# Kernel optimization log

Hardware: AMD Instinct MI355X
Metric: run time of the kernel (lower is better)

The kernel has to match this reference:

```python
import math
import jax, jax.numpy as jnp
import numpy as np

N, T, C = 4, 2048, 1024
H, HS = 16, 64  # n_head, head_size; attention_dim = H*HS = 1024
LAYER_ID, N_LAYERS = 1, 12
_EPS = math.exp(-LAYER_ID / N_LAYERS)
EPS_R = _EPS / 2.0
EPS_K = _EPS + 0.3 * LAYER_ID / (N_LAYERS - 1)
EPS_V = _EPS


def setup_inputs() -> dict:
    key = jax.random.key(0)
    ks = jax.random.split(key, 9)
    s = 1.0 / math.sqrt(C)
    return {
        "x":  jax.random.normal(ks[0], (N, T, C), dtype=jnp.float32),
        "Wr": jax.random.normal(ks[1], (H * HS, C), dtype=jnp.float32) * s,
        "br": jax.random.normal(ks[2], (H * HS,), dtype=jnp.float32) * 0.01,
        "Wk": jax.random.normal(ks[3], (H * HS, C), dtype=jnp.float32) * s,
        "bk": jax.random.normal(ks[4], (H * HS,), dtype=jnp.float32) * 0.01,
        "Wv": jax.random.normal(ks[5], (H * HS, C), dtype=jnp.float32) * s,
        "bv": jax.random.normal(ks[6], (H * HS,), dtype=jnp.float32) * 0.01,
        "Wo": jax.random.normal(ks[7], (C, H * HS), dtype=jnp.float32) * s,
        "bo": jax.random.normal(ks[8], (C,), dtype=jnp.float32) * 0.01,
        "time_decay": jnp.full((H * HS,), 0.1, dtype=jnp.float32),
        "U":          jnp.full((H * HS,), 0.1, dtype=jnp.float32),
    }


def _time_interp(x, eps):
    # eps * x[t-1] + (1-eps) * x[t+1], zero-padded at the ends (ZeroPad2d semantics)
    Tn = x.shape[1]
    curr = jnp.pad(x, ((0, 0), (1, 0), (0, 0)))[:, :Tn]   # shift right: row t <- x[t-1]
    prev = jnp.pad(x, ((0, 0), (0, 1), (0, 0)))[:, 1:]    # shift left:  row t <- x[t+1]
    return eps * curr + (1.0 - eps) * prev


def reference(x, Wr, br, Wk, bk, Wv, bv, Wo, bo, time_decay, U):
    n, t, c = x.shape
    R = (_time_interp(x, EPS_R) @ Wr.T + br).reshape(n, t, H, HS)
    K = (_time_interp(x, EPS_K) @ Wk.T + bk).reshape(n, t, H, HS)
    V = (_time_interp(x, EPS_V) @ Wv.T + bv).reshape(n, t, H, HS)

    w = jax.nn.relu(time_decay).reshape(1, 1, H, HS)
    t_rem = (t - jnp.arange(1, t + 1, dtype=x.dtype)).reshape(1, t, 1, 1)  # T-1 ... 0
    W = -w * t_rem

    e = jnp.exp(jnp.clip(W + K, -20.0, 10.0))
    past_attention = jnp.cumsum(e * V, axis=1)
    past_energy = jnp.cumsum(e, axis=1)

    shift = lambda a: jnp.pad(a, ((0, 0), (1, 0), (0, 0), (0, 0)))[:, :t]  # sum over i < t
    eu = jnp.exp(jnp.clip(U.reshape(1, 1, H, HS) + K, -20.0, 10.0))
    A = shift(past_attention) + eu * V
    B = shift(past_energy) + eu
    WKV = A / B

    out = (jax.nn.sigmoid(R) * WKV).reshape(n, t, -1) @ Wo.T + bo
    return out
```

## Files before the change

kernel.cpp:

```cpp
#include <hip/hip_runtime.h>
#include <cmath>

#define DEVFN __device__ __forceinline__

constexpr int NB = 4;
constexpr int TT = 2048;
constexpr int CD = 1024;
constexpr int MROWS = NB * TT;
constexpr int NPROJ = 3 * CD;
constexpr int NCH = 128;
constexpr int CHL = TT / NCH;

DEVFN float bf2f(unsigned short u) {
    union { unsigned int i; float f; } z; z.i = ((unsigned int)u) << 16; return z.f;
}
DEVFN unsigned short f2bf(float f) {
    union { float f; unsigned int i; } z; z.f = f;
    unsigned int r = z.i + 0x7FFFu + ((z.i >> 16) & 1u);
    return (unsigned short)(r >> 16);
}

union F4 { float4 v; float a[4]; };

DEVFN F4 ld_bf4(const unsigned short* p) {
    ushort4 u = *(const ushort4*)p;
    F4 r; r.a[0] = bf2f(u.x); r.a[1] = bf2f(u.y); r.a[2] = bf2f(u.z); r.a[3] = bf2f(u.w);
    return r;
}
DEVFN F4 zero4f() { F4 r; r.a[0] = r.a[1] = r.a[2] = r.a[3] = 0.f; return r; }

constexpr int WQ = CD * CD / 4;
constexpr int XQ = MROWS * CD / 4;
__global__ __launch_bounds__(256) void cast_all_kernel(const float* __restrict__ Wr,
                                                       const float* __restrict__ Wk,
                                                       const float* __restrict__ Wv,
                                                       const float* __restrict__ Wo,
                                                       const float* __restrict__ x,
                                                       unsigned short* __restrict__ Wcat,
                                                       unsigned short* __restrict__ Wo_bf,
                                                       unsigned short* __restrict__ xbf) {
    int i = blockIdx.x * 256 + threadIdx.x;
    const float* src; unsigned short* dst; int off;
    if (i < 3 * WQ) {
        int r = i / WQ; off = i - r * WQ;
        src = (r == 0) ? Wr : (r == 1) ? Wk : Wv;
        dst = Wcat + (size_t)r * CD * CD;
    } else if (i < 4 * WQ) {
        src = Wo; dst = Wo_bf; off = i - 3 * WQ;
    } else {
        src = x; dst = xbf; off = i - 4 * WQ;
        if (off >= XQ) return;
    }
    float4 v = ((const float4*)src)[off];
    ushort4 o;
    o.x = f2bf(v.x); o.y = f2bf(v.y); o.z = f2bf(v.z); o.w = f2bf(v.w);
    ((ushort4*)dst)[off] = o;
}

typedef __attribute__((ext_vector_type(8))) short short8;
typedef __attribute__((ext_vector_type(4))) float f32x4;

#define BM 128
#define BN 128
#define BK 64

DEVFN void store_val(float* p, float v) { *p = v; }
DEVFN void store_val(unsigned short* p, float v) { *p = f2bf(v); }

typedef const __attribute__((address_space(1))) void* gas_ptr;
typedef __attribute__((address_space(3))) void* las_ptr;

DEVFN void async_copy16(const void* g, void* l) {
    __builtin_amdgcn_global_load_lds((gas_ptr)g, (las_ptr)l, 16, 0, 0);
}

template <typename OutT>
__global__ __launch_bounds__(256) void gemm_bt(const unsigned short* __restrict__ A,
                                               const unsigned short* __restrict__ B,
                                               const float* __restrict__ bias,
                                               OutT* __restrict__ C,
                                               int M, int N, int K) {
    __shared__ __align__(16) unsigned short As[BM][BK];
    __shared__ __align__(16) unsigned short Bs[BN][BK];

    const int tid  = threadIdx.x;
    const int wave = tid >> 6;
    const int lane = tid & 63;

    const int tile_m = blockIdx.x * BM;
    const int tile_n = blockIdx.y * BN;

    const int st_row = lane >> 3;
    const int st_k   = (((lane & 7) ^ st_row) * 8);

    const int wr = wave >> 1;
    const int wc = wave & 1;
    const int lane_lo = lane & 15;
    const int lane_hi = lane >> 4;
    const int sw_m = lane_lo & 7;

    f32x4 acc[4][4];
#pragma unroll
    for (int i = 0; i < 4; i++)
#pragma unroll
        for (int j = 0; j < 4; j++) acc[i][j] = (f32x4)(0.f);

    for (int k0 = 0; k0 < K; k0 += BK) {
#pragma unroll
        for (int j = 0; j < 4; ++j) {
            int rbase = (j * 4 + wave) * 8;
            const unsigned short* gA = A + (size_t)(tile_m + rbase + st_row) * K + k0 + st_k;
            async_copy16(gA, &As[rbase][0]);
            const unsigned short* gB = B + (size_t)(tile_n + rbase + st_row) * K + k0 + st_k;
            async_copy16(gB, &Bs[rbase][0]);
        }
        __syncthreads();
#pragma unroll
        for (int ks = 0; ks < 2; ++ks) {
            short8 af[4], bf[4];
            const int kgrpA = ((ks * 4 + lane_hi) ^ sw_m) * 8;
#pragma unroll
            for (int i = 0; i < 4; i++) {
                int row = wr * 64 + i * 16 + lane_lo;
                af[i] = *(const short8*)&As[row][kgrpA];
            }
#pragma unroll
            for (int i = 0; i < 4; i++) {
                int row = wc * 64 + i * 16 + lane_lo;
                bf[i] = *(const short8*)&Bs[row][kgrpA];
            }
#pragma unroll
            for (int i = 0; i < 4; i++)
#pragma unroll
                for (int j = 0; j < 4; j++)
                    acc[i][j] = __builtin_amdgcn_mfma_f32_16x16x32_bf16(af[i], bf[j], acc[i][j], 0, 0, 0);
        }
        __syncthreads();
    }

#pragma unroll
    for (int i = 0; i < 4; i++) {
#pragma unroll
        for (int j = 0; j < 4; j++) {
            int col = tile_n + wc * 64 + j * 16 + lane_lo;
            float bv = bias ? bias[col] : 0.f;
            int row0 = tile_m + wr * 64 + i * 16 + lane_hi * 4;
#pragma unroll
            for (int r = 0; r < 4; r++) {
                store_val(&C[(size_t)(row0 + r) * N + col], acc[i][j][r] + bv);
            }
        }
    }
}

DEVFN float clip_exp(float x) { return expf(fminf(fmaxf(x, -20.f), 10.f)); }

__global__ __launch_bounds__(256) void scan_partial_kernel(const unsigned short* __restrict__ P,
                                                           const float* __restrict__ td,
                                                           const float* __restrict__ bk,
                                                           const float* __restrict__ bv,
                                                           float epsK, float epsV,
                                                           float* __restrict__ pE,
                                                           float* __restrict__ pEV) {
    const int b = blockIdx.x;
    const int n = b / NCH, ch = b % NCH;
    const int c = threadIdx.x * 4;
    const size_t RS = NPROJ;

    F4 w; w.v = *(const float4*)(td + c);
#pragma unroll
    for (int j = 0; j < 4; j++) w.a[j] = fmaxf(w.a[j], 0.f);
    F4 bk4; bk4.v = *(const float4*)(bk + c);
    F4 bv4; bv4.v = *(const float4*)(bv + c);

    const int t0 = ch * CHL;
    const unsigned short* Pk = P + (size_t)n * TT * RS + CD + c;
    const unsigned short* Pv = P + (size_t)n * TT * RS + 2 * CD + c;

    F4 km1, k0, kp1, vm1, v0, vp1;
    km1 = (t0 > 0) ? ld_bf4(Pk + (size_t)(t0 - 1) * RS) : zero4f();
    k0  = ld_bf4(Pk + (size_t)t0 * RS);
    kp1 = ld_bf4(Pk + (size_t)(t0 + 1) * RS);
    vm1 = (t0 > 0) ? ld_bf4(Pv + (size_t)(t0 - 1) * RS) : zero4f();
    v0  = ld_bf4(Pv + (size_t)t0 * RS);
    vp1 = ld_bf4(Pv + (size_t)(t0 + 1) * RS);

    const float omK = 1.f - epsK, omV = 1.f - epsV;
    float sE[4] = {0, 0, 0, 0}, sEV[4] = {0, 0, 0, 0};

#pragma unroll 4
    for (int i = 0; i < CHL; ++i) {
        const int t = t0 + i;
        const float trem = (float)(TT - 1 - t);
#pragma unroll
        for (int j = 0; j < 4; j++) {
            float kk = epsK * km1.a[j] + omK * kp1.a[j] + bk4.a[j];
            float vv = epsV * vm1.a[j] + omV * vp1.a[j] + bv4.a[j];
            float e = clip_exp(-w.a[j] * trem + kk);
            sE[j] += e;
            sEV[j] += e * vv;
        }
        km1 = k0; k0 = kp1;
        vm1 = v0; v0 = vp1;
        if (t + 2 < TT) {
            kp1 = ld_bf4(Pk + (size_t)(t + 2) * RS);
            vp1 = ld_bf4(Pv + (size_t)(t + 2) * RS);
        } else {
            kp1 = zero4f(); vp1 = zero4f();
        }
    }
    size_t pbase = ((size_t)n * NCH + ch) * CD + c;
    F4 oE, oEV;
#pragma unroll
    for (int j = 0; j < 4; j++) { oE.a[j] = sE[j]; oEV.a[j] = sEV[j]; }
    *(float4*)(pE + pbase) = oE.v;
    *(float4*)(pEV + pbase) = oEV.v;
}

__global__ __launch_bounds__(256) void scan_carry_kernel(float* __restrict__ pE,
                                                         float* __restrict__ pEV) {
    int idx = blockIdx.x * 256 + threadIdx.x;
    int n = idx / CD, c = idx % CD;
    float rE = 0.f, rEV = 0.f;
    for (int ch = 0; ch < NCH; ++ch) {
        size_t p = ((size_t)n * NCH + ch) * CD + c;
        float tE = pE[p];  pE[p]  = rE;  rE  += tE;
        float tV = pEV[p]; pEV[p] = rEV; rEV += tV;
    }
}

__global__ __launch_bounds__(256) void scan_apply_kernel(const unsigned short* __restrict__ P,
                                                         const float* __restrict__ td,
                                                         const float* __restrict__ Ub,
                                                         const float* __restrict__ br,
                                                         const float* __restrict__ bk,
                                                         const float* __restrict__ bv,
                                                         float epsR, float epsK, float epsV,
                                                         const float* __restrict__ pE,
                                                         const float* __restrict__ pEV,
                                                         unsigned short* __restrict__ gated) {
    const int b = blockIdx.x;
    const int n = b / NCH, ch = b % NCH;
    const int c = threadIdx.x * 4;
    const size_t RS = NPROJ;

    F4 w; w.v = *(const float4*)(td + c);
#pragma unroll
    for (int j = 0; j < 4; j++) w.a[j] = fmaxf(w.a[j], 0.f);
    F4 u;   u.v   = *(const float4*)(Ub + c);
    F4 br4; br4.v = *(const float4*)(br + c);
    F4 bk4; bk4.v = *(const float4*)(bk + c);
    F4 bv4; bv4.v = *(const float4*)(bv + c);

    const int t0 = ch * CHL;
    const unsigned short* Pr = P + (size_t)n * TT * RS + c;
    const unsigned short* Pk = Pr + CD;
    const unsigned short* Pv = Pr + 2 * CD;

    F4 rm1, r0, rp1, km1, k0, kp1, vm1, v0, vp1;
    rm1 = (t0 > 0) ? ld_bf4(Pr + (size_t)(t0 - 1) * RS) : zero4f();
    r0  = ld_bf4(Pr + (size_t)t0 * RS);
    rp1 = ld_bf4(Pr + (size_t)(t0 + 1) * RS);
    km1 = (t0 > 0) ? ld_bf4(Pk + (size_t)(t0 - 1) * RS) : zero4f();
    k0  = ld_bf4(Pk + (size_t)t0 * RS);
    kp1 = ld_bf4(Pk + (size_t)(t0 + 1) * RS);
    vm1 = (t0 > 0) ? ld_bf4(Pv + (size_t)(t0 - 1) * RS) : zero4f();
    v0  = ld_bf4(Pv + (size_t)t0 * RS);
    vp1 = ld_bf4(Pv + (size_t)(t0 + 1) * RS);

    size_t pbase = ((size_t)n * NCH + ch) * CD + c;
    F4 cE, cEV;
    cE.v  = *(const float4*)(pE + pbase);
    cEV.v = *(const float4*)(pEV + pbase);

    const float omR = 1.f - epsR, omK = 1.f - epsK, omV = 1.f - epsV;
    unsigned short* gbase = gated + ((size_t)n * TT + t0) * CD + c;

#pragma unroll 4
    for (int i = 0; i < CHL; ++i) {
        const int t = t0 + i;
        const float trem = (float)(TT - 1 - t);
        ushort4 og;
        unsigned short* ogp = (unsigned short*)&og;
#pragma unroll
        for (int j = 0; j < 4; j++) {
            float kk = epsK * km1.a[j] + omK * kp1.a[j] + bk4.a[j];
            float vv = epsV * vm1.a[j] + omV * vp1.a[j] + bv4.a[j];
            float rr = epsR * rm1.a[j] + omR * rp1.a[j] + br4.a[j];
            float e  = clip_exp(-w.a[j] * trem + kk);
            float eu = clip_exp(u.a[j] + kk);
            float Aj = cEV.a[j] + eu * vv;
            float Bj = cE.a[j] + eu;
            float wkv = Aj / Bj;
            float sig = 1.f / (1.f + expf(-rr));
            ogp[j] = f2bf(sig * wkv);
            cEV.a[j] += e * vv;
            cE.a[j]  += e;
        }
        *(ushort4*)(gbase + (size_t)i * CD) = og;
        rm1 = r0; r0 = rp1;
        km1 = k0; k0 = kp1;
        vm1 = v0; v0 = vp1;
        if (t + 2 < TT) {
            rp1 = ld_bf4(Pr + (size_t)(t + 2) * RS);
            kp1 = ld_bf4(Pk + (size_t)(t + 2) * RS);
            vp1 = ld_bf4(Pv + (size_t)(t + 2) * RS);
        } else {
            rp1 = zero4f(); kp1 = zero4f(); vp1 = zero4f();
        }
    }
}

extern "C" void kernel_launch(void* const* d_in, const int* in_sizes, int n_in,
                              void* d_out, int out_size, void* d_ws, size_t ws_size,
                              hipStream_t stream) {
    const float* x  = (const float*)d_in[0];
    const float* Wr = (const float*)d_in[1];
    const float* br = (const float*)d_in[2];
    const float* Wk = (const float*)d_in[3];
    const float* bk = (const float*)d_in[4];
    const float* Wv = (const float*)d_in[5];
    const float* bv = (const float*)d_in[6];
    const float* Wo = (const float*)d_in[7];
    const float* bo = (const float*)d_in[8];
    const float* td = (const float*)d_in[9];
    const float* U  = (const float*)d_in[10];
    float* out = (float*)d_out;

    const double eps0 = std::exp(-1.0 / 12.0);
    const float epsR = (float)(eps0 / 2.0);
    const float epsK = (float)(eps0 + 0.3 * 1.0 / 11.0);
    const float epsV = (float)eps0;

    char* p = (char*)d_ws;
    auto take = [&](size_t bytes) { char* q = p; p += (bytes + 255) & ~(size_t)255; return q; };
    unsigned short* Wcat_bf = (unsigned short*)take((size_t)NPROJ * CD * 2);
    unsigned short* Wo_bf   = (unsigned short*)take((size_t)CD * CD * 2);
    unsigned short* xbf     = (unsigned short*)take((size_t)MROWS * CD * 2);
    unsigned short* Pbuf    = (unsigned short*)take((size_t)MROWS * NPROJ * 2);
    float*          pE      = (float*)take((size_t)NB * NCH * CD * 4);
    float*          pEV     = (float*)take((size_t)NB * NCH * CD * 4);

    const int cast_total = 4 * WQ + XQ;
    cast_all_kernel<<<(cast_total + 255) / 256, 256, 0, stream>>>(Wr, Wk, Wv, Wo, x,
                                                                  Wcat_bf, Wo_bf, xbf);

    dim3 g1(MROWS / BM, NPROJ / BN);
    gemm_bt<unsigned short><<<g1, 256, 0, stream>>>(xbf, Wcat_bf, nullptr, Pbuf, MROWS, NPROJ, CD);

    scan_partial_kernel<<<NB * NCH, 256, 0, stream>>>(Pbuf, td, bk, bv, epsK, epsV, pE, pEV);
    scan_carry_kernel<<<(NB * CD) / 256, 256, 0, stream>>>(pE, pEV);
    scan_apply_kernel<<<NB * NCH, 256, 0, stream>>>(Pbuf, td, U, br, bk, bv, epsR, epsK, epsV,
                                                    pE, pEV, xbf);

    dim3 g2(MROWS / BM, CD / BN);
    gemm_bt<float><<<g2, 256, 0, stream>>>(xbf, Wo_bf, bo, out, MROWS, CD, CD);
}
```

Baseline: 243.2 us.

## Prefetch next GEMM K-tile into registers while computing current tile

Replaces the direct global-to-LDS async copies with register-staged loads. The next K-tile is fetched into registers before the MFMA work on the current LDS tile, then written to LDS after a barrier. This is meant to hide global load latency behind compute instead of stalling at each barrier. In exchange it uses more VGPRs and adds an explicit LDS write step.

```diff
diff --git a/kernel.cpp b/kernel.cpp
--- a/kernel.cpp
+++ b/kernel.cpp
@@ -67,13 +67,6 @@
 DEVFN void store_val(float* p, float v) { *p = v; }
 DEVFN void store_val(unsigned short* p, float v) { *p = f2bf(v); }
 
-typedef const __attribute__((address_space(1))) void* gas_ptr;
-typedef __attribute__((address_space(3))) void* las_ptr;
-
-DEVFN void async_copy16(const void* g, void* l) {
-    __builtin_amdgcn_global_load_lds((gas_ptr)g, (las_ptr)l, 16, 0, 0);
-}
-
 template <typename OutT>
 __global__ __launch_bounds__(256) void gemm_bt(const unsigned short* __restrict__ A,
                                                const unsigned short* __restrict__ B,
@@ -91,7 +84,8 @@
     const int tile_n = blockIdx.y * BN;
 
     const int st_row = lane >> 3;
-    const int st_k   = (((lane & 7) ^ st_row) * 8);
+    const int g      = lane & 7;
+    const int dst_g  = (g ^ st_row) * 8;
 
     const int wr = wave >> 1;
     const int wc = wave & 1;
@@ -99,35 +93,53 @@
     const int lane_hi = lane >> 4;
     const int sw_m = lane_lo & 7;
 
+    const unsigned short* gA = A + (size_t)(tile_m + wave * 8 + st_row) * K + g * 8;
+    const unsigned short* gB = B + (size_t)(tile_n + wave * 8 + st_row) * K + g * 8;
+    const size_t rstep = (size_t)32 * K;
+
     f32x4 acc[4][4];
 #pragma unroll
     for (int i = 0; i < 4; i++)
 #pragma unroll
         for (int j = 0; j < 4; j++) acc[i][j] = (f32x4)(0.f);
 
-    for (int k0 = 0; k0 < K; k0 += BK) {
+    short8 pa[4], pb[4];
+    auto load_tile = [&](int k0) {
 #pragma unroll
         for (int j = 0; j < 4; ++j) {
-            int rbase = (j * 4 + wave) * 8;
-            const unsigned short* gA = A + (size_t)(tile_m + rbase + st_row) * K + k0 + st_k;
-            async_copy16(gA, &As[rbase][0]);
-            const unsigned short* gB = B + (size_t)(tile_n + rbase + st_row) * K + k0 + st_k;
-            async_copy16(gB, &Bs[rbase][0]);
-        }
-        __syncthreads();
+            pa[j] = *(const short8*)(gA + j * rstep + k0);
+            pb[j] = *(const short8*)(gB + j * rstep + k0);
+        }
+    };
+    auto write_tile = [&]() {
+#pragma unroll
+        for (int j = 0; j < 4; ++j) {
+            int rbase = (j * 4 + wave) * 8 + st_row;
+            *(short8*)&As[rbase][dst_g] = pa[j];
+            *(short8*)&Bs[rbase][dst_g] = pb[j];
+        }
+    };
+
+    load_tile(0);
+    write_tile();
+    __syncthreads();
+
+    for (int k0 = BK;; k0 += BK) {
+        const bool has_next = (k0 < K);
+        if (has_next) load_tile(k0);
 #pragma unroll
         for (int ks = 0; ks < 2; ++ks) {
+            const int kgrp = ((ks * 4 + lane_hi) ^ sw_m) * 8;
             short8 af[4], bf[4];
-            const int kgrpA = ((ks * 4 + lane_hi) ^ sw_m) * 8;
 #pragma unroll
             for (int i = 0; i < 4; i++) {
                 int row = wr * 64 + i * 16 + lane_lo;
-                af[i] = *(const short8*)&As[row][kgrpA];
+                af[i] = *(const short8*)&As[row][kgrp];
             }
 #pragma unroll
             for (int i = 0; i < 4; i++) {
                 int row = wc * 64 + i * 16 + lane_lo;
-                bf[i] = *(const short8*)&Bs[row][kgrpA];
+                bf[i] = *(const short8*)&Bs[row][kgrp];
             }
 #pragma unroll
             for (int i = 0; i < 4; i++)
@@ -135,6 +147,9 @@
                 for (int j = 0; j < 4; j++)
                     acc[i][j] = __builtin_amdgcn_mfma_f32_16x16x32_bf16(af[i], bf[j], acc[i][j], 0, 0, 0);
         }
+        __syncthreads();
+        if (!has_next) break;
+        write_tile();
         __syncthreads();
     }
 
```

Result: slower. 257.8 us (+6.0%).
